# Kernel optimization log

Hardware: AMD Instinct MI355X
Metric: run time of the kernel (lower is better)

Reference implementation:

```python
import jax, jax.numpy as jnp
import numpy as np

V, H, L, S = 50257, 1024, 2, 2048

def setup_inputs() -> dict:
    key = jax.random.key(0)
    ks = jax.random.split(key, 20)
    s = 0.02
    return {
        "word_input": jax.random.randint(ks[0], (1,), 0, V),
        "last_context": jax.random.normal(ks[1], (1, H), jnp.float32),
        "last_hidden": jax.random.normal(ks[2], (L, 1, H), jnp.float32),
        "encoder_outputs": jax.random.normal(ks[3], (S, 1, H), jnp.float32),
        "emb": jax.random.normal(ks[4], (V, H), jnp.float32) * s,
        "W_ih0": jax.random.normal(ks[5], (3 * H, 2 * H), jnp.float32) * s,
        "W_hh0": jax.random.normal(ks[6], (3 * H, H), jnp.float32) * s,
        "b_ih0": jax.random.normal(ks[7], (3 * H,), jnp.float32) * s,
        "b_hh0": jax.random.normal(ks[8], (3 * H,), jnp.float32) * s,
        "W_ih1": jax.random.normal(ks[9], (3 * H, H), jnp.float32) * s,
        "W_hh1": jax.random.normal(ks[10], (3 * H, H), jnp.float32) * s,
        "b_ih1": jax.random.normal(ks[11], (3 * H,), jnp.float32) * s,
        "b_hh1": jax.random.normal(ks[12], (3 * H,), jnp.float32) * s,
        "Wa": jax.random.normal(ks[13], (H, H), jnp.float32) * s,
        "ba": jax.random.normal(ks[14], (H,), jnp.float32) * s,
        "W_out": jax.random.normal(ks[15], (V, 2 * H), jnp.float32) * s,
        "b_out": jax.random.normal(ks[16], (V,), jnp.float32) * s,
    }

def gru_cell(x, h, W_ih, W_hh, b_ih, b_hh):
    # x: [1, in], h: [1, H]; PyTorch GRUCell math
    gi = x @ W_ih.T + b_ih
    gh = h @ W_hh.T + b_hh
    i_r, i_z, i_n = jnp.split(gi, 3, axis=-1)
    h_r, h_z, h_n = jnp.split(gh, 3, axis=-1)
    r = jax.nn.sigmoid(i_r + h_r)
    z = jax.nn.sigmoid(i_z + h_z)
    n = jnp.tanh(i_n + r * h_n)
    return (1.0 - z) * n + z * h

def reference(word_input, last_context, last_hidden, encoder_outputs,
              emb, W_ih0, W_hh0, b_ih0, b_hh0, W_ih1, W_hh1, b_ih1, b_hh1,
              Wa, ba, W_out, b_out):
    # embedding lookup -> [1, H]; rnn input cat(embed, context) -> [1, 2H]
    word_embedded = emb[word_input].reshape(1, -1)
    rnn_input = jnp.concatenate([word_embedded, last_context], axis=1)
    # 2-layer GRU, single timestep
    h0 = gru_cell(rnn_input, last_hidden[0], W_ih0, W_hh0, b_ih0, b_hh0)
    h1 = gru_cell(h0, last_hidden[1], W_ih1, W_hh1, b_ih1, b_hh1)
    hidden = jnp.stack([h0, h1])          # [L, 1, H]
    rnn_output = h1                       # [1, H]
    # Luong 'general' attention over encoder outputs [S, 1, H]
    enc = encoder_outputs[:, 0, :]        # [S, H]
    energy = enc @ Wa.T + ba              # [S, H]
    scores = energy @ rnn_output[0]       # [S]
    attn_w = jax.nn.softmax(scores)       # [S]
    context = (attn_w @ enc)[None, :]     # [1, H]
    logits = jnp.concatenate([rnn_output, context], axis=1) @ W_out.T + b_out
    output = jax.nn.log_softmax(logits, axis=-1)  # [1, V]
    attn_weights = attn_w[None, None, :]  # [1, 1, S]
    return output, context, hidden, attn_weights
```

## Files before the change

### kernel.cpp

```cpp
#include <hip/hip_runtime.h>
#include <hip/hip_bf16.h>

namespace {

constexpr int V   = 50257;
constexpr int H   = 1024;
constexpr int SEQ = 2048;

__device__ __forceinline__ float dot4(const float4 p, const float* __restrict__ x) {
  return p.x * x[0] + p.y * x[1] + p.z * x[2] + p.w * x[3];
}

__device__ __forceinline__ float wred(float v) {
#pragma unroll
  for (int off = 32; off; off >>= 1) v += __shfl_xor(v, off, 64);
  return v;
}

__global__ __launch_bounds__(256) void k_gru0(
    const int* __restrict__ word, const float* __restrict__ emb,
    const float* __restrict__ last_context, const float* __restrict__ last_hidden0,
    const float* __restrict__ W_ih, const float* __restrict__ W_hh,
    const float* __restrict__ b_ih, const float* __restrict__ b_hh,
    float* __restrict__ h_ws, float* __restrict__ h_out)
{
  __shared__ float xs[2 * H];
  __shared__ float hs[H];
  const int tid = threadIdx.x;
  const size_t wrow = (size_t)word[0] * H;
  for (int i = tid; i < H; i += 256) {
    xs[i]     = emb[wrow + i];
    xs[H + i] = last_context[i];
    hs[i]     = last_hidden0[i];
  }
  __syncthreads();
  const int wave = tid >> 6, lane = tid & 63;
  const int j = blockIdx.x * 4 + wave;
  float acc[6];
#pragma unroll
  for (int g = 0; g < 3; ++g) {
    const float4* Wr = (const float4*)(W_ih + (size_t)(g * H + j) * (2 * H));
    float a = 0.f;
#pragma unroll
    for (int c = 0; c < 8; ++c)
      a += dot4(Wr[c * 64 + lane], &xs[c * 256 + lane * 4]);
    acc[g] = a;
  }
#pragma unroll
  for (int g = 0; g < 3; ++g) {
    const float4* Wr = (const float4*)(W_hh + (size_t)(g * H + j) * H);
    float a = 0.f;
#pragma unroll
    for (int c = 0; c < 4; ++c)
      a += dot4(Wr[c * 64 + lane], &hs[c * 256 + lane * 4]);
    acc[3 + g] = a;
  }
#pragma unroll
  for (int g = 0; g < 6; ++g) acc[g] = wred(acc[g]);
  if (lane == 0) {
    float gir = acc[0] + b_ih[j];
    float giz = acc[1] + b_ih[H + j];
    float gin = acc[2] + b_ih[2 * H + j];
    float ghr = acc[3] + b_hh[j];
    float ghz = acc[4] + b_hh[H + j];
    float ghn = acc[5] + b_hh[2 * H + j];
    float r = 1.f / (1.f + expf(-(gir + ghr)));
    float z = 1.f / (1.f + expf(-(giz + ghz)));
    float n = tanhf(gin + r * ghn);
    float h = (1.f - z) * n + z * hs[j];
    h_ws[j]  = h;
    h_out[j] = h;
  }
}

__global__ __launch_bounds__(256) void k_gru1(
    const float* __restrict__ x_ws, const float* __restrict__ last_hidden1,
    const float* __restrict__ W_ih, const float* __restrict__ W_hh,
    const float* __restrict__ b_ih, const float* __restrict__ b_hh,
    float* __restrict__ h_ws, float* __restrict__ h_out)
{
  __shared__ float xs[H];
  __shared__ float hs[H];
  const int tid = threadIdx.x;
  for (int i = tid; i < H; i += 256) {
    xs[i] = x_ws[i];
    hs[i] = last_hidden1[i];
  }
  __syncthreads();
  const int wave = tid >> 6, lane = tid & 63;
  const int j = blockIdx.x * 4 + wave;
  float acc[6];
#pragma unroll
  for (int g = 0; g < 3; ++g) {
    const float4* Wr = (const float4*)(W_ih + (size_t)(g * H + j) * H);
    float a = 0.f;
#pragma unroll
    for (int c = 0; c < 4; ++c)
      a += dot4(Wr[c * 64 + lane], &xs[c * 256 + lane * 4]);
    acc[g] = a;
  }
#pragma unroll
  for (int g = 0; g < 3; ++g) {
    const float4* Wr = (const float4*)(W_hh + (size_t)(g * H + j) * H);
    float a = 0.f;
#pragma unroll
    for (int c = 0; c < 4; ++c)
      a += dot4(Wr[c * 64 + lane], &hs[c * 256 + lane * 4]);
    acc[3 + g] = a;
  }
#pragma unroll
  for (int g = 0; g < 6; ++g) acc[g] = wred(acc[g]);
  if (lane == 0) {
    float gir = acc[0] + b_ih[j];
    float giz = acc[1] + b_ih[H + j];
    float gin = acc[2] + b_ih[2 * H + j];
    float ghr = acc[3] + b_hh[j];
    float ghz = acc[4] + b_hh[H + j];
    float ghn = acc[5] + b_hh[2 * H + j];
    float r = 1.f / (1.f + expf(-(gir + ghr)));
    float z = 1.f / (1.f + expf(-(giz + ghz)));
    float n = tanhf(gin + r * ghn);
    float h = (1.f - z) * n + z * hs[j];
    h_ws[j]  = h;
    h_out[j] = h;
  }
}

__global__ __launch_bounds__(256) void k_wat(
    const float* __restrict__ Wa, const float* __restrict__ h1, float* __restrict__ v)
{
  const int t = threadIdx.x, b = blockIdx.x;
  float a0 = 0.f, a1 = 0.f, a2 = 0.f, a3 = 0.f;
  for (int j = b * 16; j < b * 16 + 16; ++j) {
    float hj = h1[j];
    float4 w = ((const float4*)(Wa + (size_t)j * H))[t];
    a0 += hj * w.x;
    a1 += hj * w.y;
    a2 += hj * w.z;
    a3 += hj * w.w;
  }
  atomicAdd(&v[t * 4 + 0], a0);
  atomicAdd(&v[t * 4 + 1], a1);
  atomicAdd(&v[t * 4 + 2], a2);
  atomicAdd(&v[t * 4 + 3], a3);
}

__global__ __launch_bounds__(256) void k_scores(
    const float* __restrict__ enc, const float* __restrict__ v, float* __restrict__ sc)
{
  __shared__ float vs[H];
  const int tid = threadIdx.x;
  for (int i = tid; i < H; i += 256) vs[i] = v[i];
  __syncthreads();
  const int wave = tid >> 6, lane = tid & 63;
  const int i = blockIdx.x * 4 + wave;
  const float4* er = (const float4*)(enc + (size_t)i * H);
  float a = 0.f;
#pragma unroll
  for (int c = 0; c < 4; ++c)
    a += dot4(er[c * 64 + lane], &vs[c * 256 + lane * 4]);
  a = wred(a);
  if (lane == 0) sc[i] = a;
}

__global__ __launch_bounds__(256) void k_softmax(
    const float* __restrict__ sc, float* __restrict__ aw, float* __restrict__ aw_out)
{
  __shared__ float red[256];
  const int tid = threadIdx.x;
  float m = -1e30f;
  for (int i = tid; i < SEQ; i += 256) m = fmaxf(m, sc[i]);
  red[tid] = m; __syncthreads();
  for (int s = 128; s; s >>= 1) { if (tid < s) red[tid] = fmaxf(red[tid], red[tid + s]); __syncthreads(); }
  const float M = red[0]; __syncthreads();
  float sum = 0.f;
  for (int i = tid; i < SEQ; i += 256) sum += expf(sc[i] - M);
  red[tid] = sum; __syncthreads();
  for (int s = 128; s; s >>= 1) { if (tid < s) red[tid] += red[tid + s]; __syncthreads(); }
  const float inv = 1.f / red[0];
  for (int i = tid; i < SEQ; i += 256) {
    float w = expf(sc[i] - M) * inv;
    aw[i] = w;
    aw_out[i] = w;
  }
}

__global__ __launch_bounds__(256) void k_ctx(
    const float* __restrict__ enc, const float* __restrict__ aw, float* __restrict__ ctx)
{
  const int t = threadIdx.x, b = blockIdx.x;
  float a0 = 0.f, a1 = 0.f, a2 = 0.f, a3 = 0.f;
  for (int i = b * 16; i < b * 16 + 16; ++i) {
    float w = aw[i];
    float4 e = ((const float4*)(enc + (size_t)i * H))[t];
    a0 += w * e.x;
    a1 += w * e.y;
    a2 += w * e.z;
    a3 += w * e.w;
  }
  atomicAdd(&ctx[t * 4 + 0], a0);
  atomicAdd(&ctx[t * 4 + 1], a1);
  atomicAdd(&ctx[t * 4 + 2], a2);
  atomicAdd(&ctx[t * 4 + 3], a3);
}

__global__ __launch_bounds__(256) void k_logits(
    const float* __restrict__ h1, const float* __restrict__ ctx,
    const float* __restrict__ W_out, const float* __restrict__ b_out,
    float* __restrict__ logits)
{
  __shared__ float xs[2 * H];
  const int tid = threadIdx.x;
  for (int i = tid; i < H; i += 256) {
    xs[i]     = h1[i];
    xs[H + i] = ctx[i];
  }
  __syncthreads();
  const int wave = tid >> 6, lane = tid & 63;
  const int row = blockIdx.x * 4 + wave;
  if (row < V) {
    const float4* Wr = (const float4*)(W_out + (size_t)row * (2 * H));
    float a = 0.f;
#pragma unroll
    for (int c = 0; c < 8; ++c)
      a += dot4(Wr[c * 64 + lane], &xs[c * 256 + lane * 4]);
    a = wred(a);
    if (lane == 0) logits[row] = a + b_out[row];
  }
}

__global__ __launch_bounds__(256) void k_lse(
    const float* __restrict__ logits, float* __restrict__ lse,
    const float* __restrict__ ctx, float* __restrict__ ctx_out)
{
  __shared__ float red[256];
  const int tid = threadIdx.x;
  float m = -1e30f;
  for (int i = tid; i < V; i += 256) m = fmaxf(m, logits[i]);
  red[tid] = m; __syncthreads();
  for (int s = 128; s; s >>= 1) { if (tid < s) red[tid] = fmaxf(red[tid], red[tid + s]); __syncthreads(); }
  const float M = red[0]; __syncthreads();
  float sum = 0.f;
  for (int i = tid; i < V; i += 256) sum += expf(logits[i] - M);
  red[tid] = sum; __syncthreads();
  for (int s = 128; s; s >>= 1) { if (tid < s) red[tid] += red[tid + s]; __syncthreads(); }
  if (tid == 0) lse[0] = M + logf(red[0]);
  for (int i = tid; i < H; i += 256) ctx_out[i] = ctx[i];
}

__global__ __launch_bounds__(256) void k_out(
    const float* __restrict__ logits, const float* __restrict__ lse,
    float* __restrict__ out)
{
  const int i = blockIdx.x * 256 + threadIdx.x;
  if (i < V) out[i] = logits[i] - lse[0];
}

}

extern "C" void kernel_launch(void* const* d_in, const int* in_sizes, int n_in,
                              void* d_out, int out_size, void* d_ws, size_t ws_size,
                              hipStream_t stream)
{
  const int*   word          = (const int*)d_in[0];
  const float* last_context  = (const float*)d_in[1];
  const float* last_hidden   = (const float*)d_in[2];
  const float* enc           = (const float*)d_in[3];
  const float* emb           = (const float*)d_in[4];
  const float* W_ih0         = (const float*)d_in[5];
  const float* W_hh0         = (const float*)d_in[6];
  const float* b_ih0         = (const float*)d_in[7];
  const float* b_hh0         = (const float*)d_in[8];
  const float* W_ih1         = (const float*)d_in[9];
  const float* W_hh1         = (const float*)d_in[10];
  const float* b_ih1         = (const float*)d_in[11];
  const float* b_hh1         = (const float*)d_in[12];
  const float* Wa            = (const float*)d_in[13];
  const float* W_out         = (const float*)d_in[15];
  const float* b_out         = (const float*)d_in[16];

  float* ws = (float*)d_ws;
  float* v      = ws;
  float* ctx    = ws + 1024;
  float* h0     = ws + 2048;
  float* h1     = ws + 3072;
  float* sc     = ws + 4096;
  float* aw     = ws + 6144;
  float* logits = ws + 8192;
  float* lse    = ws + 8192 + 50260;

  float* out     = (float*)d_out;
  float* out_ctx = out + V;
  float* out_h0  = out + V + H;
  float* out_h1  = out + V + 2 * H;
  float* out_att = out + V + 3 * H;

  hipMemsetAsync(d_ws, 0, 2048 * sizeof(float), stream);

  hipLaunchKernelGGL(k_gru0, dim3(256), dim3(256), 0, stream,
                     word, emb, last_context, last_hidden,
                     W_ih0, W_hh0, b_ih0, b_hh0, h0, out_h0);
  hipLaunchKernelGGL(k_gru1, dim3(256), dim3(256), 0, stream,
                     h0, last_hidden + H, W_ih1, W_hh1, b_ih1, b_hh1, h1, out_h1);
  hipLaunchKernelGGL(k_wat, dim3(64), dim3(256), 0, stream, Wa, h1, v);
  hipLaunchKernelGGL(k_scores, dim3(SEQ / 4), dim3(256), 0, stream, enc, v, sc);
  hipLaunchKernelGGL(k_softmax, dim3(1), dim3(256), 0, stream, sc, aw, out_att);
  hipLaunchKernelGGL(k_ctx, dim3(SEQ / 16), dim3(256), 0, stream, enc, aw, ctx);
  hipLaunchKernelGGL(k_logits, dim3((V + 3) / 4), dim3(256), 0, stream,
                     h1, ctx, W_out, b_out, logits);
  hipLaunchKernelGGL(k_lse, dim3(1), dim3(256), 0, stream, logits, lse, ctx, out_ctx);
  hipLaunchKernelGGL(k_out, dim3((V + 255) / 256), dim3(256), 0, stream, logits, lse, out);
}
```

Baseline: 778.5 us.

## Fuse attention stages into cooperative kernel and parallelize log-softmax reduction

Merges the four attention kernels (Wa projection, scores, softmax, context) into one cooperative kernel separated by grid-wide syncs, which removes three launches. Computes the logits max inside the logits kernel with an order-preserving atomicMax, and replaces the single-block log-sum-exp kernel with a 64-block atomic exp-sum. The intent is to cut launch overhead and the serial single-block pass over 50K logits. In exchange it adds grid-sync cost and atomic nondeterminism, and it needs all 512 blocks to be co-resident for the cooperative launch.

```diff
diff --git a/kernel.cpp b/kernel.cpp
--- a/kernel.cpp
+++ b/kernel.cpp
@@ -1,5 +1,7 @@
 #include <hip/hip_runtime.h>
-#include <hip/hip_bf16.h>
+#include <hip/hip_cooperative_groups.h>
+
+namespace cg = cooperative_groups;
 
 namespace {
 
@@ -15,6 +17,15 @@
 #pragma unroll
   for (int off = 32; off; off >>= 1) v += __shfl_xor(v, off, 64);
   return v;
+}
+
+__device__ __forceinline__ unsigned fenc(float x) {
+  unsigned u = __float_as_uint(x);
+  return u ^ ((unsigned)((int)u >> 31) | 0x80000000u);
+}
+__device__ __forceinline__ float fdec(unsigned k) {
+  unsigned u = k ^ (((int)k >= 0) ? 0xFFFFFFFFu : 0x80000000u);
+  return __uint_as_float(u);
 }
 
 __global__ __launch_bounds__(256) void k_gru0(
@@ -126,98 +137,100 @@
   }
 }
 
-__global__ __launch_bounds__(256) void k_wat(
-    const float* __restrict__ Wa, const float* __restrict__ h1, float* __restrict__ v)
-{
-  const int t = threadIdx.x, b = blockIdx.x;
-  float a0 = 0.f, a1 = 0.f, a2 = 0.f, a3 = 0.f;
-  for (int j = b * 16; j < b * 16 + 16; ++j) {
-    float hj = h1[j];
-    float4 w = ((const float4*)(Wa + (size_t)j * H))[t];
-    a0 += hj * w.x;
-    a1 += hj * w.y;
-    a2 += hj * w.z;
-    a3 += hj * w.w;
-  }
-  atomicAdd(&v[t * 4 + 0], a0);
-  atomicAdd(&v[t * 4 + 1], a1);
-  atomicAdd(&v[t * 4 + 2], a2);
-  atomicAdd(&v[t * 4 + 3], a3);
-}
-
-__global__ __launch_bounds__(256) void k_scores(
-    const float* __restrict__ enc, const float* __restrict__ v, float* __restrict__ sc)
-{
+__global__ __launch_bounds__(256) void k_attn(
+    const float* __restrict__ Wa, const float* __restrict__ enc,
+    const float* __restrict__ h1, float* __restrict__ v,
+    float* __restrict__ sc, float* __restrict__ aw,
+    float* __restrict__ aw_out, float* __restrict__ ctx)
+{
+  cg::grid_group grid = cg::this_grid();
   __shared__ float vs[H];
-  const int tid = threadIdx.x;
+  __shared__ float red[256];
+  const int tid = threadIdx.x;
+  const int b   = blockIdx.x;
+
+  if (b < 64) {
+    float a0 = 0.f, a1 = 0.f, a2 = 0.f, a3 = 0.f;
+    for (int j = b * 16; j < b * 16 + 16; ++j) {
+      float hj = h1[j];
+      float4 w = ((const float4*)(Wa + (size_t)j * H))[tid];
+      a0 += hj * w.x; a1 += hj * w.y; a2 += hj * w.z; a3 += hj * w.w;
+    }
+    atomicAdd(&v[tid * 4 + 0], a0);
+    atomicAdd(&v[tid * 4 + 1], a1);
+    atomicAdd(&v[tid * 4 + 2], a2);
+    atomicAdd(&v[tid * 4 + 3], a3);
+  }
+  grid.sync();
+
   for (int i = tid; i < H; i += 256) vs[i] = v[i];
   __syncthreads();
-  const int wave = tid >> 6, lane = tid & 63;
-  const int i = blockIdx.x * 4 + wave;
-  const float4* er = (const float4*)(enc + (size_t)i * H);
-  float a = 0.f;
-#pragma unroll
-  for (int c = 0; c < 4; ++c)
-    a += dot4(er[c * 64 + lane], &vs[c * 256 + lane * 4]);
-  a = wred(a);
-  if (lane == 0) sc[i] = a;
-}
-
-__global__ __launch_bounds__(256) void k_softmax(
-    const float* __restrict__ sc, float* __restrict__ aw, float* __restrict__ aw_out)
-{
-  __shared__ float red[256];
-  const int tid = threadIdx.x;
-  float m = -1e30f;
-  for (int i = tid; i < SEQ; i += 256) m = fmaxf(m, sc[i]);
-  red[tid] = m; __syncthreads();
-  for (int s = 128; s; s >>= 1) { if (tid < s) red[tid] = fmaxf(red[tid], red[tid + s]); __syncthreads(); }
-  const float M = red[0]; __syncthreads();
-  float sum = 0.f;
-  for (int i = tid; i < SEQ; i += 256) sum += expf(sc[i] - M);
-  red[tid] = sum; __syncthreads();
-  for (int s = 128; s; s >>= 1) { if (tid < s) red[tid] += red[tid + s]; __syncthreads(); }
-  const float inv = 1.f / red[0];
-  for (int i = tid; i < SEQ; i += 256) {
-    float w = expf(sc[i] - M) * inv;
-    aw[i] = w;
-    aw_out[i] = w;
-  }
-}
-
-__global__ __launch_bounds__(256) void k_ctx(
-    const float* __restrict__ enc, const float* __restrict__ aw, float* __restrict__ ctx)
-{
-  const int t = threadIdx.x, b = blockIdx.x;
-  float a0 = 0.f, a1 = 0.f, a2 = 0.f, a3 = 0.f;
-  for (int i = b * 16; i < b * 16 + 16; ++i) {
-    float w = aw[i];
-    float4 e = ((const float4*)(enc + (size_t)i * H))[t];
-    a0 += w * e.x;
-    a1 += w * e.y;
-    a2 += w * e.z;
-    a3 += w * e.w;
-  }
-  atomicAdd(&ctx[t * 4 + 0], a0);
-  atomicAdd(&ctx[t * 4 + 1], a1);
-  atomicAdd(&ctx[t * 4 + 2], a2);
-  atomicAdd(&ctx[t * 4 + 3], a3);
+  {
+    const int wave = tid >> 6, lane = tid & 63;
+    const int i = b * 4 + wave;
+    const float4* er = (const float4*)(enc + (size_t)i * H);
+    float a = 0.f;
+#pragma unroll
+    for (int c = 0; c < 4; ++c)
+      a += dot4(er[c * 64 + lane], &vs[c * 256 + lane * 4]);
+    a = wred(a);
+    if (lane == 0) sc[i] = a;
+  }
+  grid.sync();
+
+  if (b == 0) {
+    float m = -1e30f;
+    for (int k = tid; k < SEQ; k += 256) m = fmaxf(m, sc[k]);
+    red[tid] = m; __syncthreads();
+    for (int s = 128; s; s >>= 1) { if (tid < s) red[tid] = fmaxf(red[tid], red[tid + s]); __syncthreads(); }
+    const float M = red[0]; __syncthreads();
+    float sum = 0.f;
+    for (int k = tid; k < SEQ; k += 256) sum += expf(sc[k] - M);
+    red[tid] = sum; __syncthreads();
+    for (int s = 128; s; s >>= 1) { if (tid < s) red[tid] += red[tid + s]; __syncthreads(); }
+    const float inv = 1.f / red[0];
+    for (int k = tid; k < SEQ; k += 256) {
+      float w = expf(sc[k] - M) * inv;
+      aw[k] = w;
+      aw_out[k] = w;
+    }
+  }
+  grid.sync();
+
+  if (b < 128) {
+    float a0 = 0.f, a1 = 0.f, a2 = 0.f, a3 = 0.f;
+    for (int k = b * 16; k < b * 16 + 16; ++k) {
+      float w = aw[k];
+      float4 e = ((const float4*)(enc + (size_t)k * H))[tid];
+      a0 += w * e.x; a1 += w * e.y; a2 += w * e.z; a3 += w * e.w;
+    }
+    atomicAdd(&ctx[tid * 4 + 0], a0);
+    atomicAdd(&ctx[tid * 4 + 1], a1);
+    atomicAdd(&ctx[tid * 4 + 2], a2);
+    atomicAdd(&ctx[tid * 4 + 3], a3);
+  }
 }
 
 __global__ __launch_bounds__(256) void k_logits(
     const float* __restrict__ h1, const float* __restrict__ ctx,
     const float* __restrict__ W_out, const float* __restrict__ b_out,
-    float* __restrict__ logits)
+    float* __restrict__ logits, unsigned* __restrict__ maxkey,
+    float* __restrict__ ctx_out)
 {
   __shared__ float xs[2 * H];
+  __shared__ float wmax[4];
   const int tid = threadIdx.x;
   for (int i = tid; i < H; i += 256) {
     xs[i]     = h1[i];
     xs[H + i] = ctx[i];
   }
   __syncthreads();
+  if (blockIdx.x == 0) {
+    for (int i = tid; i < H; i += 256) ctx_out[i] = xs[H + i];
+  }
   const int wave = tid >> 6, lane = tid & 63;
   const int row = blockIdx.x * 4 + wave;
+  float val = -3.0e38f;
   if (row < V) {
     const float4* Wr = (const float4*)(W_out + (size_t)row * (2 * H));
     float a = 0.f;
@@ -225,35 +238,41 @@
     for (int c = 0; c < 8; ++c)
       a += dot4(Wr[c * 64 + lane], &xs[c * 256 + lane * 4]);
     a = wred(a);
-    if (lane == 0) logits[row] = a + b_out[row];
-  }
-}
-
-__global__ __launch_bounds__(256) void k_lse(
-    const float* __restrict__ logits, float* __restrict__ lse,
-    const float* __restrict__ ctx, float* __restrict__ ctx_out)
+    if (lane == 0) {
+      val = a + b_out[row];
+      logits[row] = val;
+    }
+  }
+  if (lane == 0) wmax[wave] = val;
+  __syncthreads();
+  if (tid == 0) {
+    float m = fmaxf(fmaxf(wmax[0], wmax[1]), fmaxf(wmax[2], wmax[3]));
+    atomicMax(maxkey, fenc(m));
+  }
+}
+
+__global__ __launch_bounds__(256) void k_lse_sum(
+    const float* __restrict__ logits, const unsigned* __restrict__ maxkey,
+    float* __restrict__ expsum)
 {
   __shared__ float red[256];
   const int tid = threadIdx.x;
-  float m = -1e30f;
-  for (int i = tid; i < V; i += 256) m = fmaxf(m, logits[i]);
-  red[tid] = m; __syncthreads();
-  for (int s = 128; s; s >>= 1) { if (tid < s) red[tid] = fmaxf(red[tid], red[tid + s]); __syncthreads(); }
-  const float M = red[0]; __syncthreads();
-  float sum = 0.f;
-  for (int i = tid; i < V; i += 256) sum += expf(logits[i] - M);
-  red[tid] = sum; __syncthreads();
-  for (int s = 128; s; s >>= 1) { if (tid < s) red[tid] += red[tid + s]; __syncthreads(); }
-  if (tid == 0) lse[0] = M + logf(red[0]);
-  for (int i = tid; i < H; i += 256) ctx_out[i] = ctx[i];
+  const float M = fdec(*maxkey);
+  float s = 0.f;
+  for (int i = blockIdx.x * 256 + tid; i < V; i += 64 * 256)
+    s += expf(logits[i] - M);
+  red[tid] = s; __syncthreads();
+  for (int st = 128; st; st >>= 1) { if (tid < st) red[tid] += red[tid + st]; __syncthreads(); }
+  if (tid == 0) atomicAdd(expsum, red[0]);
 }
 
 __global__ __launch_bounds__(256) void k_out(
-    const float* __restrict__ logits, const float* __restrict__ lse,
-    float* __restrict__ out)
+    const float* __restrict__ logits, const unsigned* __restrict__ maxkey,
+    const float* __restrict__ expsum, float* __restrict__ out)
 {
   const int i = blockIdx.x * 256 + threadIdx.x;
-  if (i < V) out[i] = logits[i] - lse[0];
+  const float lse = fdec(*maxkey) + logf(*expsum);
+  if (i < V) out[i] = logits[i] - lse;
 }
 
 }
@@ -280,14 +299,15 @@
   const float* b_out         = (const float*)d_in[16];
 
   float* ws = (float*)d_ws;
-  float* v      = ws;
-  float* ctx    = ws + 1024;
-  float* h0     = ws + 2048;
-  float* h1     = ws + 3072;
-  float* sc     = ws + 4096;
-  float* aw     = ws + 6144;
-  float* logits = ws + 8192;
-  float* lse    = ws + 8192 + 50260;
+  float*    v      = ws;
+  float*    ctx    = ws + 1024;
+  unsigned* maxkey = (unsigned*)(ws + 2048);
+  float*    expsum = ws + 2049;
+  float*    h0     = ws + 2560;
+  float*    h1     = ws + 3584;
+  float*    sc     = ws + 4608;
+  float*    aw     = ws + 6656;
+  float*    logits = ws + 8704;
 
   float* out     = (float*)d_out;
   float* out_ctx = out + V;
@@ -295,19 +315,26 @@
   float* out_h1  = out + V + 2 * H;
   float* out_att = out + V + 3 * H;
 
-  hipMemsetAsync(d_ws, 0, 2048 * sizeof(float), stream);
+  hipMemsetAsync(d_ws, 0, 2304 * sizeof(float), stream);
 
   hipLaunchKernelGGL(k_gru0, dim3(256), dim3(256), 0, stream,
                      word, emb, last_context, last_hidden,
                      W_ih0, W_hh0, b_ih0, b_hh0, h0, out_h0);
   hipLaunchKernelGGL(k_gru1, dim3(256), dim3(256), 0, stream,
                      h0, last_hidden + H, W_ih1, W_hh1, b_ih1, b_hh1, h1, out_h1);
-  hipLaunchKernelGGL(k_wat, dim3(64), dim3(256), 0, stream, Wa, h1, v);
-  hipLaunchKernelGGL(k_scores, dim3(SEQ / 4), dim3(256), 0, stream, enc, v, sc);
-  hipLaunchKernelGGL(k_softmax, dim3(1), dim3(256), 0, stream, sc, aw, out_att);
-  hipLaunchKernelGGL(k_ctx, dim3(SEQ / 16), dim3(256), 0, stream, enc, aw, ctx);
+
+  {
+    void* attn_args[] = {
+      (void*)&Wa, (void*)&enc, (void*)&h1, (void*)&v,
+      (void*)&sc, (void*)&aw, (void*)&out_att, (void*)&ctx };
+    hipLaunchCooperativeKernel((void*)k_attn, dim3(512), dim3(256),
+                               attn_args, 0, stream);
+  }
+
   hipLaunchKernelGGL(k_logits, dim3((V + 3) / 4), dim3(256), 0, stream,
-                     h1, ctx, W_out, b_out, logits);
-  hipLaunchKernelGGL(k_lse, dim3(1), dim3(256), 0, stream, logits, lse, ctx, out_ctx);
-  hipLaunchKernelGGL(k_out, dim3((V + 255) / 256), dim3(256), 0, stream, logits, lse, out);
-}
+                     h1, ctx, W_out, b_out, logits, maxkey, out_ctx);
+  hipLaunchKernelGGL(k_lse_sum, dim3(64), dim3(256), 0, stream,
+                     logits, maxkey, expsum);
+  hipLaunchKernelGGL(k_out, dim3((V + 255) / 256), dim3(256), 0, stream,
+                     logits, maxkey, expsum, out);
+}
```

Result: slower. 954.3 us (+22.6%).
